# Kernel optimization log

Measured on AMD Instinct MI355X. Metric: run time of the kernel, lower is better.

Reference implementation:

```python
import jax, jax.numpy as jnp
import numpy as np
from jax.scipy.special import gammaln, digamma, polygamma

B, K = 8192, 128
LAMBDA_KL = 1.0
LAMBDA_LOGDET = 0.01
JITTER = 1e-6


def setup_inputs() -> dict:
    key = jax.random.key(0)
    k1, k2 = jax.random.split(key)
    # Dirichlet concentrations must be > 0
    alpha = jax.random.uniform(k1, (B, K), jnp.float32, 0.5, 5.0)
    target = jax.random.randint(k2, (B,), 0, K)
    return {"alpha": alpha, "target": target}


def _fisher_diag(alpha):
    # trigamma(alpha_i) - trigamma(S)
    s = alpha.sum(axis=1, keepdims=True)
    return polygamma(1, alpha) - polygamma(1, s)


def reference(alpha, target):
    bsz, k = alpha.shape
    dtype = alpha.dtype
    s = alpha.sum(axis=1, keepdims=True)          # [B,1]
    y = jax.nn.one_hot(target, k, dtype=dtype)    # [B,K]

    # ---- i_mse (Fisher-weighted Brier) ----
    p = alpha / s
    err = (y - p) ** 2
    var = p * (1.0 - p) / (s + 1.0)
    w = jnp.clip(_fisher_diag(alpha), 1e-8)       # clamp_min
    i_mse = (w * (err + var)).sum(axis=1).mean()

    # ---- KL( Dir(alpha_hat) || Dir(1) ) ----
    alpha_hat = alpha * (1.0 - y) + y             # evidence removed at true class
    s_hat = alpha_hat.sum(axis=1)                 # [B]
    kl_ps = (gammaln(s_hat)
             - gammaln(jnp.asarray(float(k), dtype))
             - gammaln(alpha_hat).sum(axis=1)
             + ((alpha_hat - 1.0)
                * (digamma(alpha_hat) - digamma(s_hat)[:, None])).sum(axis=1))
    kl = kl_ps.mean()

    # ---- log|FIM|, FIM = diag(trigamma(alpha)) - trigamma(S) * 11^T ----
    trig = polygamma(1, alpha)                    # [B,K]
    trig_s = polygamma(1, alpha.sum(axis=1))      # [B]
    eye = jnp.eye(k, dtype=dtype)
    fim = trig[:, :, None] * eye - trig_s[:, None, None] + JITTER * eye  # [B,K,K]
    sign, logabsdet = jnp.linalg.slogdet(fim)
    logdet_ps = jnp.where(sign > 0, logabsdet, jnp.full_like(logabsdet, -20.0))
    logdet_mean = logdet_ps.mean()

    total = i_mse + LAMBDA_KL * kl - LAMBDA_LOGDET * logdet_mean
    return (total, i_mse, kl, logdet_mean)
```

## Files before the change

### kernel.cpp

```cpp
#include <hip/hip_runtime.h>
#include <hip/hip_bf16.h>
#include <math.h>

#define B_ROWS 8192
#define K_DIM  128
#define LAMBDA_KL 1.0f
#define LAMBDA_LOGDET 0.01f
#define JITTER 1e-6f

__device__ __forceinline__ float rcpf(float x) { return __builtin_amdgcn_rcpf(x); }

__device__ __forceinline__ void special3(float x, float& dg, float& tg, float& lg) {
    const float x1 = x + 1.f, x2 = x + 2.f, x3 = x + 3.f, x4 = x + 4.f, x5 = x + 5.f;
    const float r0 = rcpf(x),  r1 = rcpf(x1), r2 = rcpf(x2);
    const float r3 = rcpf(x3), r4 = rcpf(x4), r5 = rcpf(x5);
    const float y  = x + 6.f;
    const float iy = rcpf(y);
    const float f  = iy * iy;
    const float ly = __logf(y);

    const float dg_y = ly - 0.5f * iy
                     + f * (-1.f/12.f + f * (1.f/120.f + f * (-1.f/252.f)));
    dg = dg_y - (((r0 + r1) + (r2 + r3)) + (r4 + r5));

    const float tg_y = iy * (1.f + iy * (0.5f + iy * (1.f/6.f
                     + f * (-1.f/30.f + f * (1.f/42.f)))));
    tg = tg_y + (((r0*r0 + r1*r1) + (r2*r2 + r3*r3)) + (r4*r4 + r5*r5));

    const float lg_y = (y - 0.5f) * ly - y + 0.91893853320467274f
                     + iy * (1.f/12.f + f * (-1.f/360.f + f * (1.f/1260.f)));
    const float prod = ((x * x1) * (x2 * x3)) * (x4 * x5);
    lg = lg_y - __logf(prod);
}

__device__ __forceinline__ float digamma_big(float y) {
    const float iy = rcpf(y), f = iy * iy;
    return __logf(y) - 0.5f * iy - f * (1.f/12.f);
}
__device__ __forceinline__ float trigamma_big(float y) {
    const float iy = rcpf(y), f = iy * iy;
    return iy + 0.5f * f + f * iy * (1.f/6.f);
}
__device__ __forceinline__ float lgamma_big(float y) {
    const float iy = rcpf(y);
    return (y - 0.5f) * __logf(y) - y + 0.91893853320467274f + iy * (1.f/12.f);
}

__global__ __launch_bounds__(256)
void iedl_row_kernel(const float* __restrict__ alpha,
                     const int* __restrict__ target,
                     float* __restrict__ ws) {
    const int wave = threadIdx.x >> 6;
    const int lane = threadIdx.x & 63;
    const int b    = blockIdx.x * 4 + wave;

    const float2 a2 = ((const float2*)(alpha + (size_t)b * K_DIM))[lane];
    const int    tgt = target[b];

    float s = a2.x + a2.y;
    #pragma unroll
    for (int m = 1; m < 64; m <<= 1) s += __shfl_xor(s, m);

    const float a_pick = (tgt & 1) ? a2.y : a2.x;
    const float a_t    = __shfl(a_pick, tgt >> 1);

    const float s_hat  = s - a_t + 1.f;
    const float trig_s = trigamma_big(s);
    const float dg_sh  = digamma_big(s_hat);
    const float inv_s  = rcpf(s);
    const float inv_s1 = rcpf(s + 1.f);

    float mse_sum = 0.f, kl_sum = 0.f, logd_sum = 0.f, invd_sum = 0.f;

    #pragma unroll
    for (int e = 0; e < 2; ++e) {
        const int   k  = 2 * lane + e;
        const float ad = (e == 0) ? a2.x : a2.y;

        float dg_a, tg_a, lg_a;
        special3(ad, dg_a, tg_a, lg_a);

        const float p   = ad * inv_s;
        const float y1  = (k == tgt) ? 1.f : 0.f;
        const float err = (y1 - p) * (y1 - p);
        const float var = p * (1.f - p) * inv_s1;
        const float w   = fmaxf(tg_a - trig_s, 1e-8f);
        mse_sum += w * (err + var);

        if (k != tgt) kl_sum += -lg_a + (ad - 1.f) * (dg_a - dg_sh);

        const float D = tg_a + JITTER;
        logd_sum += __logf(D);
        invd_sum += rcpf(D);
    }

    #pragma unroll
    for (int m = 1; m < 64; m <<= 1) {
        mse_sum  += __shfl_xor(mse_sum,  m);
        kl_sum   += __shfl_xor(kl_sum,   m);
        logd_sum += __shfl_xor(logd_sum, m);
        invd_sum += __shfl_xor(invd_sum, m);
    }

    if (lane == 0) {
        const float kl_row = lgamma_big(s_hat) - 491.5534482f + kl_sum;
        const float t = 1.f - trig_s * invd_sum;
        const float logdet_row = (t > 0.f) ? (logd_sum + __logf(t)) : -20.f;
        ws[b]              = mse_sum;
        ws[B_ROWS + b]     = kl_row;
        ws[2 * B_ROWS + b] = logdet_row;
    }
}

__global__ __launch_bounds__(1024)
void iedl_reduce_kernel(const float* __restrict__ ws, float* __restrict__ out) {
    const int tid = threadIdx.x;
    float m = 0.f, k = 0.f, l = 0.f;
    #pragma unroll
    for (int i = 0; i < B_ROWS / 1024; ++i) {
        const int idx = tid + i * 1024;
        m += ws[idx];
        k += ws[B_ROWS + idx];
        l += ws[2 * B_ROWS + idx];
    }
    double md = m, kd = k, ld = l;
    #pragma unroll
    for (int off = 1; off < 64; off <<= 1) {
        md += __shfl_xor(md, off);
        kd += __shfl_xor(kd, off);
        ld += __shfl_xor(ld, off);
    }
    __shared__ double sm[3][16];
    const int wid = tid >> 6;
    if ((tid & 63) == 0) { sm[0][wid] = md; sm[1][wid] = kd; sm[2][wid] = ld; }
    __syncthreads();
    if (tid == 0) {
        double M = 0.0, KK = 0.0, L = 0.0;
        #pragma unroll
        for (int w = 0; w < 16; ++w) { M += sm[0][w]; KK += sm[1][w]; L += sm[2][w]; }
        const double inv_b = 1.0 / (double)B_ROWS;
        const double i_mse = M * inv_b;
        const double kl    = KK * inv_b;
        const double ldm   = L * inv_b;
        out[0] = (float)(i_mse + (double)LAMBDA_KL * kl - (double)LAMBDA_LOGDET * ldm);
        out[1] = (float)i_mse;
        out[2] = (float)kl;
        out[3] = (float)ldm;
    }
}

extern "C" void kernel_launch(void* const* d_in, const int* in_sizes, int n_in,
                              void* d_out, int out_size, void* d_ws, size_t ws_size,
                              hipStream_t stream) {
    const float* alpha  = (const float*)d_in[0];
    const int*   target = (const int*)d_in[1];
    float*       out    = (float*)d_out;
    float*       ws     = (float*)d_ws;

    iedl_row_kernel<<<B_ROWS / 4, 256, 0, stream>>>(alpha, target, ws);
    iedl_reduce_kernel<<<1, 1024, 0, stream>>>(ws, out);
}
```

Baseline: 63.72 us.

## Fuse row and reduction kernels with last-block atomic-counter finalization

Merges the per-row kernel and the single-block reduction kernel into one launch. Each wave now processes four rows and accumulates locally, each block writes one partial, and the last block to arrive (found through an atomic counter) does the final double-precision reduction. This removes the second kernel launch and the large per-row workspace traffic. In exchange it adds a memset before the launch and uses fewer, larger blocks, which may lower latency hiding.

```diff
diff --git a/kernel.cpp b/kernel.cpp
--- a/kernel.cpp
+++ b/kernel.cpp
@@ -2,11 +2,13 @@
 #include <hip/hip_bf16.h>
 #include <math.h>
 
-#define B_ROWS 8192
-#define K_DIM  128
-#define LAMBDA_KL 1.0f
-#define LAMBDA_LOGDET 0.01f
-#define JITTER 1e-6f
+#define B_ROWS   8192
+#define K_DIM    128
+#define NBLOCKS  256
+#define NTHREADS 512
+#define NWAVES   8
+#define ROWS_PER_WAVE 4
+#define JITTER   1e-6f
 
 __device__ __forceinline__ float rcpf(float x) { return __builtin_amdgcn_rcpf(x); }
 
@@ -46,106 +48,122 @@
     return (y - 0.5f) * __logf(y) - y + 0.91893853320467274f + iy * (1.f/12.f);
 }
 
-__global__ __launch_bounds__(256)
-void iedl_row_kernel(const float* __restrict__ alpha,
-                     const int* __restrict__ target,
-                     float* __restrict__ ws) {
+__global__ __launch_bounds__(NTHREADS)
+void iedl_fused(const float* __restrict__ alpha,
+                const int* __restrict__ target,
+                float* __restrict__ ws,
+                float* __restrict__ out) {
     const int wave = threadIdx.x >> 6;
     const int lane = threadIdx.x & 63;
-    const int b    = blockIdx.x * 4 + wave;
 
-    const float2 a2 = ((const float2*)(alpha + (size_t)b * K_DIM))[lane];
-    const int    tgt = target[b];
+    float acc_mse = 0.f, acc_kl = 0.f, acc_ld = 0.f;
 
-    float s = a2.x + a2.y;
+    const int row0 = blockIdx.x * (NWAVES * ROWS_PER_WAVE) + wave * ROWS_PER_WAVE;
     #pragma unroll
-    for (int m = 1; m < 64; m <<= 1) s += __shfl_xor(s, m);
+    for (int r = 0; r < ROWS_PER_WAVE; ++r) {
+        const int b = row0 + r;
+        const float2 a2 = ((const float2*)(alpha + (size_t)b * K_DIM))[lane];
+        const int tgt = target[b];
 
-    const float a_pick = (tgt & 1) ? a2.y : a2.x;
-    const float a_t    = __shfl(a_pick, tgt >> 1);
+        float s = a2.x + a2.y;
+        #pragma unroll
+        for (int m = 1; m < 64; m <<= 1) s += __shfl_xor(s, m);
 
-    const float s_hat  = s - a_t + 1.f;
-    const float trig_s = trigamma_big(s);
-    const float dg_sh  = digamma_big(s_hat);
-    const float inv_s  = rcpf(s);
-    const float inv_s1 = rcpf(s + 1.f);
+        const float a_pick = (tgt & 1) ? a2.y : a2.x;
+        const float a_t    = __shfl(a_pick, tgt >> 1);
 
-    float mse_sum = 0.f, kl_sum = 0.f, logd_sum = 0.f, invd_sum = 0.f;
+        const float s_hat  = s - a_t + 1.f;
+        const float trig_s = trigamma_big(s);
+        const float dg_sh  = digamma_big(s_hat);
+        const float inv_s  = rcpf(s);
+        const float inv_s1 = rcpf(s + 1.f);
 
-    #pragma unroll
-    for (int e = 0; e < 2; ++e) {
-        const int   k  = 2 * lane + e;
-        const float ad = (e == 0) ? a2.x : a2.y;
+        float mse_sum = 0.f, kl_sum = 0.f, logd_sum = 0.f, invd_sum = 0.f;
+        #pragma unroll
+        for (int e = 0; e < 2; ++e) {
+            const int   k  = 2 * lane + e;
+            const float ad = (e == 0) ? a2.x : a2.y;
 
-        float dg_a, tg_a, lg_a;
-        special3(ad, dg_a, tg_a, lg_a);
+            float dg_a, tg_a, lg_a;
+            special3(ad, dg_a, tg_a, lg_a);
 
-        const float p   = ad * inv_s;
-        const float y1  = (k == tgt) ? 1.f : 0.f;
-        const float err = (y1 - p) * (y1 - p);
-        const float var = p * (1.f - p) * inv_s1;
-        const float w   = fmaxf(tg_a - trig_s, 1e-8f);
-        mse_sum += w * (err + var);
+            const float p   = ad * inv_s;
+            const float y1  = (k == tgt) ? 1.f : 0.f;
+            const float err = (y1 - p) * (y1 - p);
+            const float var = p * (1.f - p) * inv_s1;
+            const float w   = fmaxf(tg_a - trig_s, 1e-8f);
+            mse_sum += w * (err + var);
 
-        if (k != tgt) kl_sum += -lg_a + (ad - 1.f) * (dg_a - dg_sh);
+            if (k != tgt) kl_sum += -lg_a + (ad - 1.f) * (dg_a - dg_sh);
 
-        const float D = tg_a + JITTER;
-        logd_sum += __logf(D);
-        invd_sum += rcpf(D);
+            const float D = tg_a + JITTER;
+            logd_sum += __logf(D);
+            invd_sum += rcpf(D);
+        }
+
+        #pragma unroll
+        for (int m = 1; m < 64; m <<= 1) {
+            mse_sum  += __shfl_xor(mse_sum,  m);
+            kl_sum   += __shfl_xor(kl_sum,   m);
+            logd_sum += __shfl_xor(logd_sum, m);
+            invd_sum += __shfl_xor(invd_sum, m);
+        }
+
+        acc_mse += mse_sum;
+        acc_kl  += lgamma_big(s_hat) - 491.5534482f + kl_sum;
+        const float t = 1.f - trig_s * invd_sum;
+        acc_ld  += (t > 0.f) ? (logd_sum + __logf(t)) : -20.f;
     }
 
-    #pragma unroll
-    for (int m = 1; m < 64; m <<= 1) {
-        mse_sum  += __shfl_xor(mse_sum,  m);
-        kl_sum   += __shfl_xor(kl_sum,   m);
-        logd_sum += __shfl_xor(logd_sum, m);
-        invd_sum += __shfl_xor(invd_sum, m);
+    __shared__ float sm[3][NWAVES];
+    __shared__ int   is_last;
+    if (lane == 0) { sm[0][wave] = acc_mse; sm[1][wave] = acc_kl; sm[2][wave] = acc_ld; }
+    __syncthreads();
+
+    unsigned* counter = (unsigned*)ws;
+    float*    part    = ws + 32;
+
+    if (threadIdx.x == 0) {
+        float M = 0.f, KK = 0.f, L = 0.f;
+        #pragma unroll
+        for (int w = 0; w < NWAVES; ++w) { M += sm[0][w]; KK += sm[1][w]; L += sm[2][w]; }
+        __hip_atomic_store(&part[blockIdx.x],               M,  __ATOMIC_RELAXED, __HIP_MEMORY_SCOPE_AGENT);
+        __hip_atomic_store(&part[NBLOCKS + blockIdx.x],     KK, __ATOMIC_RELAXED, __HIP_MEMORY_SCOPE_AGENT);
+        __hip_atomic_store(&part[2 * NBLOCKS + blockIdx.x], L,  __ATOMIC_RELAXED, __HIP_MEMORY_SCOPE_AGENT);
+        const unsigned old = __hip_atomic_fetch_add(counter, 1u, __ATOMIC_ACQ_REL, __HIP_MEMORY_SCOPE_AGENT);
+        is_last = (old == NBLOCKS - 1) ? 1 : 0;
     }
+    __syncthreads();
 
-    if (lane == 0) {
-        const float kl_row = lgamma_big(s_hat) - 491.5534482f + kl_sum;
-        const float t = 1.f - trig_s * invd_sum;
-        const float logdet_row = (t > 0.f) ? (logd_sum + __logf(t)) : -20.f;
-        ws[b]              = mse_sum;
-        ws[B_ROWS + b]     = kl_row;
-        ws[2 * B_ROWS + b] = logdet_row;
-    }
-}
-
-__global__ __launch_bounds__(1024)
-void iedl_reduce_kernel(const float* __restrict__ ws, float* __restrict__ out) {
-    const int tid = threadIdx.x;
-    float m = 0.f, k = 0.f, l = 0.f;
-    #pragma unroll
-    for (int i = 0; i < B_ROWS / 1024; ++i) {
-        const int idx = tid + i * 1024;
-        m += ws[idx];
-        k += ws[B_ROWS + idx];
-        l += ws[2 * B_ROWS + idx];
-    }
-    double md = m, kd = k, ld = l;
-    #pragma unroll
-    for (int off = 1; off < 64; off <<= 1) {
-        md += __shfl_xor(md, off);
-        kd += __shfl_xor(kd, off);
-        ld += __shfl_xor(ld, off);
-    }
-    __shared__ double sm[3][16];
-    const int wid = tid >> 6;
-    if ((tid & 63) == 0) { sm[0][wid] = md; sm[1][wid] = kd; sm[2][wid] = ld; }
-    __syncthreads();
-    if (tid == 0) {
-        double M = 0.0, KK = 0.0, L = 0.0;
+    if (is_last) {
+        double m = 0.0, k = 0.0, l = 0.0;
+        if (threadIdx.x < NBLOCKS) {
+            m = (double)__hip_atomic_load(&part[threadIdx.x],               __ATOMIC_RELAXED, __HIP_MEMORY_SCOPE_AGENT);
+            k = (double)__hip_atomic_load(&part[NBLOCKS + threadIdx.x],     __ATOMIC_RELAXED, __HIP_MEMORY_SCOPE_AGENT);
+            l = (double)__hip_atomic_load(&part[2 * NBLOCKS + threadIdx.x], __ATOMIC_RELAXED, __HIP_MEMORY_SCOPE_AGENT);
+        }
         #pragma unroll
-        for (int w = 0; w < 16; ++w) { M += sm[0][w]; KK += sm[1][w]; L += sm[2][w]; }
-        const double inv_b = 1.0 / (double)B_ROWS;
-        const double i_mse = M * inv_b;
-        const double kl    = KK * inv_b;
-        const double ldm   = L * inv_b;
-        out[0] = (float)(i_mse + (double)LAMBDA_KL * kl - (double)LAMBDA_LOGDET * ldm);
-        out[1] = (float)i_mse;
-        out[2] = (float)kl;
-        out[3] = (float)ldm;
+        for (int off = 1; off < 64; off <<= 1) {
+            m += __shfl_xor(m, off);
+            k += __shfl_xor(k, off);
+            l += __shfl_xor(l, off);
+        }
+        __shared__ double dsm[3][NWAVES];
+        if (lane == 0) { dsm[0][wave] = m; dsm[1][wave] = k; dsm[2][wave] = l; }
+        __syncthreads();
+        if (threadIdx.x == 0) {
+            double M = 0.0, KK = 0.0, L = 0.0;
+            #pragma unroll
+            for (int w = 0; w < NWAVES; ++w) { M += dsm[0][w]; KK += dsm[1][w]; L += dsm[2][w]; }
+            const double inv_b = 1.0 / (double)B_ROWS;
+            const double i_mse = M * inv_b;
+            const double kl    = KK * inv_b;
+            const double ldm   = L * inv_b;
+            out[0] = (float)(i_mse + kl - 0.01 * ldm);
+            out[1] = (float)i_mse;
+            out[2] = (float)kl;
+            out[3] = (float)ldm;
+        }
     }
 }
 
@@ -157,6 +175,6 @@
     float*       out    = (float*)d_out;
     float*       ws     = (float*)d_ws;
 
-    iedl_row_kernel<<<B_ROWS / 4, 256, 0, stream>>>(alpha, target, ws);
-    iedl_reduce_kernel<<<1, 1024, 0, stream>>>(ws, out);
+    hipMemsetAsync(d_ws, 0, 128, stream);
+    iedl_fused<<<NBLOCKS, NTHREADS, 0, stream>>>(alpha, target, ws, out);
 }
```

Result: slower. 67.67 us (+6.2%).
